# Kernel optimization log

Measured on AMD Instinct MI355X. Metric: run time of the kernel, lower is better.

Reference implementation:

```python
import jax, jax.numpy as jnp
import numpy as np

N = 50000
E = 800000
IN_CH = 512
OUT_CH = 64
ITERATIONS = 3  # adjacency power order; iterations-1 spmm steps


def setup_inputs() -> dict:
    key = jax.random.key(0)
    k1, k2, k3, k4, k5 = jax.random.split(key, 5)
    adj_indices = jax.random.randint(k1, (2, E), 0, N, dtype=jnp.int32)
    adj_values = jax.random.uniform(k2, (E,), dtype=jnp.float32)
    features = jax.random.normal(k3, (N, IN_CH), dtype=jnp.float32)
    # xavier-uniform init bounds
    bw = float(np.sqrt(6.0 / (IN_CH + OUT_CH)))
    weight = jax.random.uniform(k4, (IN_CH, OUT_CH), minval=-bw, maxval=bw, dtype=jnp.float32)
    bb = float(np.sqrt(6.0 / (1 + OUT_CH)))
    bias = jax.random.uniform(k5, (1, OUT_CH), minval=-bb, maxval=bb, dtype=jnp.float32)
    return {"adj_indices": adj_indices, "adj_values": adj_values,
            "features": features, "weight": weight, "bias": bias}


def reference(adj_indices, adj_values, features, weight, bias):
    # dense projection: [N, in] @ [in, out] -> [N, out]
    x = features @ weight
    # dropout is identity in eval mode (training=False)
    row, col = adj_indices[0], adj_indices[1]
    # (iterations - 1) sparse-dense matmuls: x <- A @ x
    for _ in range(ITERATIONS - 1):
        gathered = adj_values[:, None] * x[col]          # [E, out]
        x = jax.ops.segment_sum(gathered, row, num_segments=N)
    return x + bias
```

## Files before the change

kernel.cpp:

```cpp
#include <hip/hip_runtime.h>
#include <hip/hip_bf16.h>
#include <hip/hip_fp16.h>

#define NN 50000
#define INCH 512
#define OUTCH 64
#define NTILES 3125
#define MAXD 48
#define GB 782
#define SCB 1024
#define RPB 32
#define NBUCKET 1563
#define NPART 8
#define BCAPP 112
#define TSTR 16

typedef __attribute__((ext_vector_type(8))) short short8;
typedef __attribute__((ext_vector_type(4))) float floatx4;
typedef unsigned long long u64;

__device__ __forceinline__ unsigned packbf2(float a, float b) {
    __hip_bfloat162 h = __float22bfloat162_rn(make_float2(a, b));
    unsigned r;
    __builtin_memcpy(&r, &h, 4);
    return r;
}
__device__ __forceinline__ unsigned short f2bf(float f) {
    unsigned u = __float_as_uint(f);
    return (unsigned short)((u + 0x7FFFu + ((u >> 16) & 1u)) >> 16);
}
__device__ __forceinline__ float bf2f(unsigned short u) {
    return __uint_as_float(((unsigned)u) << 16);
}

__global__ __launch_bounds__(256) void prep_kernel(const float* __restrict__ W,
                                                   unsigned short* __restrict__ Wbf,
                                                   int* __restrict__ btail) {
    const int i = blockIdx.x * 256 + threadIdx.x;
    if (i < (NBUCKET * NPART * TSTR) / 4)
        *reinterpret_cast<uint4*>(btail + i * 4) = uint4{0u, 0u, 0u, 0u};
    if (i < INCH * OUTCH) {
        const int k = i >> 6;
        const int n = i & 63;
        Wbf[n * INCH + k] = f2bf(W[i]);
    }
}

__global__ __launch_bounds__(256, 4) void gemm_kernel(
        const float* __restrict__ A, const unsigned short* __restrict__ Wbf,
        unsigned short* __restrict__ C) {
    __shared__ unsigned short ldsT[4][16 * 64];
    const int t = threadIdx.x;
    const int lane = t & 63;
    const int wave = t >> 6;
    const int tile = blockIdx.x * 4 + wave;
    if (tile >= NTILES) return;
    const int rbase = tile * 16;
    const int frow = lane & 15;
    const int quad = lane >> 4;
    const float* Ap = A + (size_t)(rbase + frow) * INCH + quad * 8;
    const unsigned short* Bp = Wbf + frow * INCH + quad * 8;

    floatx4 acc[4] = {floatx4{0,0,0,0}, floatx4{0,0,0,0}, floatx4{0,0,0,0}, floatx4{0,0,0,0}};

#pragma unroll
    for (int c = 0; c < 16; ++c) {
        const float4 a0 = *(const float4*)(Ap + c * 32);
        const float4 a1 = *(const float4*)(Ap + c * 32 + 4);
        short8 bfr[4];
#pragma unroll
        for (int f = 0; f < 4; ++f)
            bfr[f] = *(const short8*)(Bp + (size_t)f * 16 * INCH + c * 32);
        uint4 au;
        au.x = packbf2(a0.x, a0.y);
        au.y = packbf2(a0.z, a0.w);
        au.z = packbf2(a1.x, a1.y);
        au.w = packbf2(a1.z, a1.w);
        const short8 af = *(const short8*)&au;
#pragma unroll
        for (int f = 0; f < 4; ++f)
            acc[f] = __builtin_amdgcn_mfma_f32_16x16x32_bf16(af, bfr[f], acc[f], 0, 0, 0);
    }

    unsigned short* myT = ldsT[wave];
#pragma unroll
    for (int f = 0; f < 4; ++f)
#pragma unroll
        for (int reg = 0; reg < 4; ++reg)
            myT[(quad * 4 + reg) * 64 + f * 16 + frow] = f2bf(acc[f][reg]);
    unsigned short* Cw = C + (size_t)rbase * OUTCH;
#pragma unroll
    for (int it = 0; it < 2; ++it) {
        const short8 v = *(const short8*)&myT[it * 512 + lane * 8];
        *(short8*)(Cw + it * 512 + lane * 8) = v;
    }
}

__global__ __launch_bounds__(256) void scatter_kernel(
        const int* __restrict__ rows, const int* __restrict__ cols,
        const float* __restrict__ vals, int* __restrict__ btail,
        u64* __restrict__ buckets, int E_) {
    const int part = blockIdx.x & 7;
    for (int e = blockIdx.x * 256 + threadIdx.x; e < E_; e += SCB * 256) {
        const int r = __builtin_nontemporal_load(rows + e);
        const int c = __builtin_nontemporal_load(cols + e);
        const float v = __builtin_nontemporal_load(vals + e);
        const unsigned short hv = __half_as_ushort(__float2half(v));
        const u64 rec = (u64)(unsigned)(r & 0xFFFF)
                      | ((u64)(unsigned)(c & 0xFFFF) << 16)
                      | ((u64)hv << 32);
        const int sb = (r >> 5) * NPART + part;
        const int pos = atomicAdd(&btail[sb * TSTR], 1);
        if (pos < BCAPP)
            buckets[(size_t)sb * BCAPP + pos] = rec;
    }
}

__global__ __launch_bounds__(256) void bucketize(
        const int* __restrict__ btail, const u64* __restrict__ buckets,
        unsigned* __restrict__ ell, int* __restrict__ deg) {
    __shared__ int cnt[RPB];
    __shared__ __align__(16) unsigned stage[RPB * MAXD];
    const int t = threadIdx.x;
    const int b = blockIdx.x;

    if (t < RPB) cnt[t] = 0;
    for (int j = t; j < RPB * MAXD; j += 256) stage[j] = 0u;
    __syncthreads();

    for (int part = 0; part < NPART; ++part) {
        const int sb = b * NPART + part;
        int n = btail[sb * TSTR];
        n = n < BCAPP ? n : BCAPP;
        const u64* base = buckets + (size_t)sb * BCAPP;
        for (int i = t; i < n; i += 256) {
            const u64 rec = __builtin_nontemporal_load(base + i);
            const int rloc = (int)rec & 31;
            const int slot = atomicAdd(&cnt[rloc], 1);
            if (slot < MAXD)
                stage[rloc * MAXD + slot] = (unsigned)(rec >> 16);
        }
    }
    __syncthreads();

    uint4* dst = (uint4*)(ell + (size_t)b * RPB * MAXD);
    const uint4* src = (const uint4*)stage;
    for (int j = t; j < (RPB * MAXD) / 4; j += 256) dst[j] = src[j];
    const int row = b * RPB + t;
    if (t < RPB && row < NN) {
        int d = cnt[t];
        deg[row] = d < MAXD ? d : MAXD;
    }
}

template <bool LAST>
__global__ __launch_bounds__(256) void spmm_full(const int* __restrict__ deg,
                                                 const unsigned* __restrict__ ell,
                                                 const unsigned short* __restrict__ xin,
                                                 void* __restrict__ xout_,
                                                 const float* __restrict__ bias) {
    const int t = threadIdx.x;
    const int lane = t & 63;
    const int eslot = lane >> 3;
    const int cg = lane & 7;
    const int row = blockIdx.x * 4 + (t >> 6);
    int d = deg[row];
    d = d < MAXD ? d : MAXD;
    const unsigned* eb = ell + (size_t)row * MAXD;

    unsigned p[6];
#pragma unroll
    for (int j = 0; j < 6; ++j)
        p[j] = __builtin_nontemporal_load(eb + eslot + 8 * j);
#pragma unroll
    for (int j = 0; j < 6; ++j)
        if (eslot + 8 * j >= d) p[j] = 0u;

    const unsigned short* xh = xin + cg * 8;
    float acc[8] = {0.f, 0.f, 0.f, 0.f, 0.f, 0.f, 0.f, 0.f};

#pragma unroll
    for (int j = 0; j < 6; ++j) {
        if (d > 8 * j) {
            const unsigned P = p[j];
            const short8 xv = *(const short8*)(xh + (size_t)(P & 0xFFFFu) * OUTCH);
            const float v = __half2float(__ushort_as_half((unsigned short)(P >> 16)));
#pragma unroll
            for (int k = 0; k < 8; ++k)
                acc[k] = fmaf(v, bf2f((unsigned short)xv[k]), acc[k]);
        }
    }

#pragma unroll
    for (int k = 0; k < 8; ++k) {
        acc[k] += __shfl_xor(acc[k], 8, 64);
        acc[k] += __shfl_xor(acc[k], 16, 64);
        acc[k] += __shfl_xor(acc[k], 32, 64);
    }

    if (eslot == 0) {
        const int chb = cg * 8;
        if (LAST) {
            float* op = (float*)xout_ + (size_t)row * OUTCH + chb;
            const floatx4 b0 = *(const floatx4*)(bias + chb);
            const floatx4 b1 = *(const floatx4*)(bias + chb + 4);
            floatx4 o0, o1;
            o0[0] = acc[0] + b0[0]; o0[1] = acc[1] + b0[1];
            o0[2] = acc[2] + b0[2]; o0[3] = acc[3] + b0[3];
            o1[0] = acc[4] + b1[0]; o1[1] = acc[5] + b1[1];
            o1[2] = acc[6] + b1[2]; o1[3] = acc[7] + b1[3];
            __builtin_nontemporal_store(o0, (floatx4*)op);
            __builtin_nontemporal_store(o1, (floatx4*)(op + 4));
        } else {
            unsigned short* op = (unsigned short*)xout_ + (size_t)row * OUTCH + chb;
            short8 o;
#pragma unroll
            for (int k = 0; k < 8; ++k) o[k] = (short)f2bf(acc[k]);
            *(short8*)op = o;
        }
    }
}

extern "C" void kernel_launch(void* const* d_in, const int* in_sizes, int n_in,
                              void* d_out, int out_size, void* d_ws, size_t ws_size,
                              hipStream_t stream) {
    const int*   adj   = (const int*)d_in[0];
    const float* avals = (const float*)d_in[1];
    const float* feat  = (const float*)d_in[2];
    const float* W     = (const float*)d_in[3];
    const float* bias  = (const float*)d_in[4];
    float* out = (float*)d_out;

    const int E_ = in_sizes[1];
    const int* rows = adj;
    const int* cols = adj + E_;

    unsigned short* x0  = (unsigned short*)d_ws;
    unsigned short* x1  = x0 + (size_t)NN * OUTCH;
    unsigned short* Wbf = x1 + (size_t)NN * OUTCH;
    unsigned* ell = (unsigned*)(Wbf + (size_t)OUTCH * INCH);
    u64* buckets = (u64*)(ell + (size_t)NBUCKET * RPB * MAXD);
    int* btail = (int*)(buckets + (size_t)NBUCKET * NPART * BCAPP);
    int* deg = btail + NBUCKET * NPART * TSTR;

    prep_kernel<<<196, 256, 0, stream>>>(W, Wbf, btail);

    gemm_kernel<<<GB, 256, 0, stream>>>(feat, Wbf, x0);

    scatter_kernel<<<SCB, 256, 0, stream>>>(rows, cols, avals, btail, buckets, E_);

    bucketize<<<NBUCKET, 256, 0, stream>>>(btail, buckets, ell, deg);

    spmm_full<false><<<NN / 4, 256, 0, stream>>>(deg, ell, x0, x1, nullptr);
    spmm_full<true><<<NN / 4, 256, 0, stream>>>(deg, ell, x1, out, bias);
}
```

Baseline: 266.6 us.

## Stage edge records in LDS per block before flushing to coarse global buckets

The edge scatter now uses 128 blocks that each bin their edges into 391 coarse buckets of 128 rows, held in shared memory (about 125 KB). Bucket counts are then flushed to global buckets with one atomic per bucket, and overflow records fall back to per-edge global atomics. The intent is to cut global atomic contention and scattered small writes. The bucketize pass now handles 128 rows per 512-thread block from a single bucket. The risks are low occupancy in the scatter, serial per-thread flush loops, and dropped edges if a bucket exceeds its 2400-record capacity.

```diff
diff --git a/kernel.cpp b/kernel.cpp
--- a/kernel.cpp
+++ b/kernel.cpp
@@ -8,11 +8,11 @@
 #define NTILES 3125
 #define MAXD 48
 #define GB 782
-#define SCB 1024
-#define RPB 32
-#define NBUCKET 1563
-#define NPART 8
-#define BCAPP 112
+#define SCB 128
+#define RPB 128
+#define NB 391
+#define LCAP 40
+#define BCAP 2400
 #define TSTR 16
 
 typedef __attribute__((ext_vector_type(8))) short short8;
@@ -35,10 +35,10 @@
 
 __global__ __launch_bounds__(256) void prep_kernel(const float* __restrict__ W,
                                                    unsigned short* __restrict__ Wbf,
-                                                   int* __restrict__ btail) {
+                                                   int* __restrict__ gtail) {
     const int i = blockIdx.x * 256 + threadIdx.x;
-    if (i < (NBUCKET * NPART * TSTR) / 4)
-        *reinterpret_cast<uint4*>(btail + i * 4) = uint4{0u, 0u, 0u, 0u};
+    if (i < (NB * TSTR + 3) / 4)
+        *reinterpret_cast<uint4*>(gtail + i * 4) = uint4{0u, 0u, 0u, 0u};
     if (i < INCH * OUTCH) {
         const int k = i >> 6;
         const int n = i & 63;
@@ -96,12 +96,19 @@
     }
 }
 
-__global__ __launch_bounds__(256) void scatter_kernel(
+__global__ __launch_bounds__(256, 1) void scatter_chunked(
         const int* __restrict__ rows, const int* __restrict__ cols,
-        const float* __restrict__ vals, int* __restrict__ btail,
-        u64* __restrict__ buckets, int E_) {
-    const int part = blockIdx.x & 7;
-    for (int e = blockIdx.x * 256 + threadIdx.x; e < E_; e += SCB * 256) {
+        const float* __restrict__ vals, int* __restrict__ gtail,
+        u64* __restrict__ gbuckets, int E_) {
+    extern __shared__ char ldsraw[];
+    u64* lstage = (u64*)ldsraw;
+    int* lcnt = (int*)(lstage + (size_t)NB * LCAP);
+    const int t = threadIdx.x;
+
+    for (int j = t; j < NB; j += 256) lcnt[j] = 0;
+    __syncthreads();
+
+    for (int e = blockIdx.x * 256 + t; e < E_; e += SCB * 256) {
         const int r = __builtin_nontemporal_load(rows + e);
         const int c = __builtin_nontemporal_load(cols + e);
         const float v = __builtin_nontemporal_load(vals + e);
@@ -109,15 +116,32 @@
         const u64 rec = (u64)(unsigned)(r & 0xFFFF)
                       | ((u64)(unsigned)(c & 0xFFFF) << 16)
                       | ((u64)hv << 32);
-        const int sb = (r >> 5) * NPART + part;
-        const int pos = atomicAdd(&btail[sb * TSTR], 1);
-        if (pos < BCAPP)
-            buckets[(size_t)sb * BCAPP + pos] = rec;
-    }
-}
-
-__global__ __launch_bounds__(256) void bucketize(
-        const int* __restrict__ btail, const u64* __restrict__ buckets,
+        const int b = r >> 7;
+        const int pos = atomicAdd(&lcnt[b], 1);
+        if (pos < LCAP) {
+            lstage[(size_t)b * LCAP + pos] = rec;
+        } else {
+            const int gp = atomicAdd(&gtail[b * TSTR], 1);
+            if (gp < BCAP) gbuckets[(size_t)b * BCAP + gp] = rec;
+        }
+    }
+    __syncthreads();
+
+    for (int j = t; j < NB; j += 256) {
+        int n = lcnt[j];
+        n = n < LCAP ? n : LCAP;
+        if (n > 0) {
+            const int pos = atomicAdd(&gtail[j * TSTR], n);
+            u64* dst = gbuckets + (size_t)j * BCAP;
+            const u64* src = lstage + (size_t)j * LCAP;
+            for (int k = 0; k < n; ++k)
+                if (pos + k < BCAP) dst[pos + k] = src[k];
+        }
+    }
+}
+
+__global__ __launch_bounds__(512) void bucketize(
+        const int* __restrict__ gtail, const u64* __restrict__ gbuckets,
         unsigned* __restrict__ ell, int* __restrict__ deg) {
     __shared__ int cnt[RPB];
     __shared__ __align__(16) unsigned stage[RPB * MAXD];
@@ -125,31 +149,28 @@
     const int b = blockIdx.x;
 
     if (t < RPB) cnt[t] = 0;
-    for (int j = t; j < RPB * MAXD; j += 256) stage[j] = 0u;
-    __syncthreads();
-
-    for (int part = 0; part < NPART; ++part) {
-        const int sb = b * NPART + part;
-        int n = btail[sb * TSTR];
-        n = n < BCAPP ? n : BCAPP;
-        const u64* base = buckets + (size_t)sb * BCAPP;
-        for (int i = t; i < n; i += 256) {
-            const u64 rec = __builtin_nontemporal_load(base + i);
-            const int rloc = (int)rec & 31;
-            const int slot = atomicAdd(&cnt[rloc], 1);
-            if (slot < MAXD)
-                stage[rloc * MAXD + slot] = (unsigned)(rec >> 16);
-        }
-    }
-    __syncthreads();
-
+    for (int j = t; j < RPB * MAXD; j += 512) stage[j] = 0u;
+    __syncthreads();
+
+    int n = gtail[b * TSTR];
+    n = n < BCAP ? n : BCAP;
+    const u64* base = gbuckets + (size_t)b * BCAP;
+    for (int i = t; i < n; i += 512) {
+        const u64 rec = __builtin_nontemporal_load(base + i);
+        const int rloc = (int)rec & 127;
+        const int slot = atomicAdd(&cnt[rloc], 1);
+        if (slot < MAXD)
+            stage[rloc * MAXD + slot] = (unsigned)(rec >> 16);
+    }
+    __syncthreads();
+
+    const int nrows = (NN - b * RPB) < RPB ? (NN - b * RPB) : RPB;
     uint4* dst = (uint4*)(ell + (size_t)b * RPB * MAXD);
     const uint4* src = (const uint4*)stage;
-    for (int j = t; j < (RPB * MAXD) / 4; j += 256) dst[j] = src[j];
-    const int row = b * RPB + t;
-    if (t < RPB && row < NN) {
+    for (int j = t; j < (nrows * MAXD) / 4; j += 512) dst[j] = src[j];
+    if (t < nrows) {
         int d = cnt[t];
-        deg[row] = d < MAXD ? d : MAXD;
+        deg[b * RPB + t] = d < MAXD ? d : MAXD;
     }
 }
 
@@ -239,17 +260,19 @@
     unsigned short* x1  = x0 + (size_t)NN * OUTCH;
     unsigned short* Wbf = x1 + (size_t)NN * OUTCH;
     unsigned* ell = (unsigned*)(Wbf + (size_t)OUTCH * INCH);
-    u64* buckets = (u64*)(ell + (size_t)NBUCKET * RPB * MAXD);
-    int* btail = (int*)(buckets + (size_t)NBUCKET * NPART * BCAPP);
-    int* deg = btail + NBUCKET * NPART * TSTR;
-
-    prep_kernel<<<196, 256, 0, stream>>>(W, Wbf, btail);
+    u64* gbuckets = (u64*)(ell + (size_t)NN * MAXD);
+    int* gtail = (int*)(gbuckets + (size_t)NB * BCAP);
+    int* deg = gtail + NB * TSTR;
+
+    prep_kernel<<<128, 256, 0, stream>>>(W, Wbf, gtail);
 
     gemm_kernel<<<GB, 256, 0, stream>>>(feat, Wbf, x0);
 
-    scatter_kernel<<<SCB, 256, 0, stream>>>(rows, cols, avals, btail, buckets, E_);
-
-    bucketize<<<NBUCKET, 256, 0, stream>>>(btail, buckets, ell, deg);
+    const size_t scatter_lds = (size_t)NB * LCAP * sizeof(u64) + NB * sizeof(int);
+    scatter_chunked<<<SCB, 256, scatter_lds, stream>>>(rows, cols, avals,
+                                                       gtail, gbuckets, E_);
+
+    bucketize<<<NB, 512, 0, stream>>>(gtail, gbuckets, ell, deg);
 
     spmm_full<false><<<NN / 4, 256, 0, stream>>>(deg, ell, x0, x1, nullptr);
     spmm_full<true><<<NN / 4, 256, 0, stream>>>(deg, ell, x1, out, bias);
```

Result: faster. 250.6 us (-6.0%).
